# Optimization experiments

Hardware: AMD Instinct MI355X
Metric: run time of the kernel (lower is better)

## Reference

```python
import jax, jax.numpy as jnp
import numpy as np

BS = 4096
FD = 768   # feature_dim
PD = 500   # proj_dim
ZD = 300   # z_dim
R = 10     # retrieval_num
U = 10     # retrieval_user_num
N_PER = 3 + 2 * R + U  # 33 nodes per sample


def _lin(x, w, b):
    return x @ w.T + b


def _build_incidence(bs, r, u):
    # Faithful to get_hyper_edge_index_and_weight: 4 group edges per sample
    # plus R pair edges that (as in the original code) omit the batch bias,
    # i.e. always reference sample-0 nodes. dhg.Hypergraph dedups duplicate
    # edges, so the R pair edges appear once.
    n = 3 + 2 * r + u
    node_list, edge_list = [], []
    e = 0
    for b in range(bs):
        o = b * n
        groups = [
            list(range(o, o + 3)),
            list(range(o + 3, o + 3 + r)) + [o],
            list(range(o + 3 + r, o + 3 + 2 * r)) + [o + 1],
            list(range(o + 3 + 2 * r, o + n)) + [o + 2],
        ]
        for g in groups:
            node_list.extend(g)
            edge_list.extend([e] * len(g))
            e += 1
    for i in range(r):
        node_list.extend([3 + i, 3 + r + i])
        edge_list.extend([e, e])
        e += 1
    return np.asarray(node_list, np.int32), np.asarray(edge_list, np.int32), e


def setup_inputs() -> dict:
    key = jax.random.key(0)
    ks = jax.random.split(key, 32)

    def rn(k, shape, s=1.0):
        return jax.random.normal(k, shape, dtype=jnp.float32) * s

    inp = {
        "visual_feature": rn(ks[0], (BS, 1, FD)),
        "textual_feature": rn(ks[1], (BS, 1, FD)),
        "similarity": rn(ks[2], (BS, R)),
        "retrieved_visual_feature": rn(ks[3], (BS, R, 1, FD)),
        "retrieved_textual_feature": rn(ks[4], (BS, R, FD)),
        "retrieved_label": jax.random.uniform(ks[5], (BS, R, 1), dtype=jnp.float32),
        "user": rn(ks[6], (BS, FD)),
        "retrieved_user": rn(ks[7], (BS, U, FD)),
        "retrieved_user_similarity": rn(ks[8], (BS, U)),
        # learned params (0.02-scaled normal init)
        "vis_w": rn(ks[9], (PD, FD), 0.02), "vis_b": jnp.zeros((PD,), jnp.float32),
        "txt_w": rn(ks[10], (PD, FD), 0.02), "txt_b": jnp.zeros((PD,), jnp.float32),
        "usr_w": rn(ks[11], (PD, FD), 0.02), "usr_b": jnp.zeros((PD,), jnp.float32),
        "rvis_w": rn(ks[12], (PD, FD), 0.02), "rvis_b": jnp.zeros((PD,), jnp.float32),
        "rtxt_w": rn(ks[13], (PD, FD), 0.02), "rtxt_b": jnp.zeros((PD,), jnp.float32),
        "rusr_w": rn(ks[14], (PD, FD), 0.02), "rusr_b": jnp.zeros((PD,), jnp.float32),
        "hg_w": rn(ks[15], (ZD, PD), 0.02), "hg_b": jnp.zeros((ZD,), jnp.float32),
        "lbl_w": rn(ks[16], (ZD, 1), 0.02), "lbl_b": jnp.zeros((ZD,), jnp.float32),
        "p1_w": rn(ks[17], (800, ZD * 7), 0.02), "p1_b": jnp.zeros((800,), jnp.float32),
        "p2_w": rn(ks[18], (200, 800), 0.02), "p2_b": jnp.zeros((200,), jnp.float32),
        "p3_w": rn(ks[19], (1, 200), 0.02), "p3_b": jnp.zeros((1,), jnp.float32),
    }
    return inp


def reference(visual_feature, textual_feature, similarity, retrieved_visual_feature,
              retrieved_textual_feature, retrieved_label, user, retrieved_user,
              retrieved_user_similarity,
              vis_w, vis_b, txt_w, txt_b, usr_w, usr_b,
              rvis_w, rvis_b, rtxt_w, rtxt_b, rusr_w, rusr_b,
              hg_w, hg_b, lbl_w, lbl_b,
              p1_w, p1_b, p2_w, p2_b, p3_w, p3_b):
    bs = visual_feature.shape[0]
    # dense tanh embeddings -> per-sample node feature block [bs, 33, 500]
    t = jnp.tanh(_lin(textual_feature, txt_w, txt_b))
    v = jnp.tanh(_lin(visual_feature, vis_w, vis_b))
    u = jnp.tanh(_lin(user[:, None, :], usr_w, usr_b))
    rt = jnp.tanh(_lin(retrieved_textual_feature, rtxt_w, rtxt_b))
    rv = jnp.tanh(_lin(retrieved_visual_feature[:, :, 0, :], rvis_w, rvis_b))
    ru = jnp.tanh(_lin(retrieved_user, rusr_w, rusr_b))
    X = jnp.concatenate([t, v, u, rt, rv, ru], axis=1).reshape(-1, PD)  # [bs*33, 500]

    # hypergraph conv (HGNN+ layer, softmax_then_sum over unit incidence == mean)
    node_ids, edge_ids, E = _build_incidence(bs, R, U)  # static, built at trace time
    N = X.shape[0]
    Xt = _lin(X, hg_w, hg_b)  # theta: [N, 300]
    ones = jnp.ones(node_ids.shape[0], jnp.float32)
    deg_e = jax.ops.segment_sum(ones, edge_ids, num_segments=E)
    Y = jax.ops.segment_sum(Xt[node_ids], edge_ids, num_segments=E) / deg_e[:, None]
    deg_v = jax.ops.segment_sum(ones, node_ids, num_segments=N)
    Xo = jax.ops.segment_sum(Y[edge_ids], node_ids, num_segments=N) / deg_v[:, None]
    Xo = jax.nn.relu(Xo).reshape(bs, N_PER, ZD)

    # retrieval aggregation: softmax-weighted sums over retrieved sets
    sim = jax.nn.softmax(similarity, axis=1)                      # [bs, R]
    usim = jax.nn.softmax(retrieved_user_similarity, axis=1)      # [bs, U]
    rt_agg = jnp.einsum('br,brd->bd', sim, Xo[:, 3:3 + R, :])
    rv_agg = jnp.einsum('br,brd->bd', sim, Xo[:, 3 + R:3 + 2 * R, :])
    ru_agg = jnp.einsum('br,brd->bd', usim, Xo[:, 3 + 2 * R:3 + 2 * R + U, :])
    lbl_agg = jnp.einsum('br,bro->bo', sim, retrieved_label)      # [bs, 1]
    lbl_emb = jax.nn.relu(_lin(lbl_agg, lbl_w, lbl_b))            # [bs, 300]

    feat = jnp.concatenate(
        [Xo[:, 0, :], Xo[:, 1, :], Xo[:, 2, :], rv_agg, rt_agg, ru_agg, lbl_emb], axis=1)
    h = jax.nn.relu(_lin(feat, p1_w, p1_b))
    h = jax.nn.relu(_lin(h, p2_w, p2_b))
    out = jax.nn.sigmoid(_lin(h, p3_w, p3_b))  # [bs, 1]
    return out
```

## Files before the change

kernel.cpp:

```cpp
#include <hip/hip_runtime.h>
#include <math.h>

#define BS 4096
#define FD 768
#define PD 500
#define ZD 300
#define RNUM 10

typedef short bf16x8 __attribute__((ext_vector_type(8)));
typedef float f32x4 __attribute__((ext_vector_type(4)));

__device__ __forceinline__ unsigned int fbits(float f) {
  union { float f; unsigned int u; } v; v.f = f; return v.u;
}

__device__ __forceinline__ unsigned int pack2bf(float f0, float f1) {
  unsigned int u0 = fbits(f0) + 0x8000u;
  unsigned int u1 = fbits(f1) + 0x8000u;
  return __builtin_amdgcn_perm(u1, u0, 0x07060302u);
}

#define BM 128
#define BN 64
#define BK 16
#define TM 8
#define TN 4
template <int ACT>
__global__ __launch_bounds__(256) void gemm_kernel(
    const float* __restrict__ A, const float* __restrict__ W,
    const float* __restrict__ bias, float* __restrict__ C,
    int M, int N, int K) {
  __shared__ float As[BK][BM + 4];
  __shared__ float Bs[BK][BN + 4];
  const int m0 = blockIdx.x * BM;
  const int n0 = blockIdx.y * BN;
  const int tid = threadIdx.x;
  const int tx = tid & 15;
  const int ty = tid >> 4;
  float acc[TM][TN];
#pragma unroll
  for (int i = 0; i < TM; i++)
#pragma unroll
    for (int j = 0; j < TN; j++) acc[i][j] = 0.f;
  const int l_row = tid >> 2;
  const int l_k4 = (tid & 3) * 4;
  for (int k0 = 0; k0 < K; k0 += BK) {
#pragma unroll
    for (int half = 0; half < 2; ++half) {
      int m = m0 + l_row + half * 64;
      int k = k0 + l_k4;
      float4 v = make_float4(0.f, 0.f, 0.f, 0.f);
      if (m < M && k + 4 <= K) v = *(const float4*)(A + (size_t)m * K + k);
      As[l_k4 + 0][l_row + half * 64] = v.x;
      As[l_k4 + 1][l_row + half * 64] = v.y;
      As[l_k4 + 2][l_row + half * 64] = v.z;
      As[l_k4 + 3][l_row + half * 64] = v.w;
    }
    {
      int n = n0 + l_row;
      int k = k0 + l_k4;
      float4 v = make_float4(0.f, 0.f, 0.f, 0.f);
      if (n < N && k + 4 <= K) v = *(const float4*)(W + (size_t)n * K + k);
      Bs[l_k4 + 0][l_row] = v.x;
      Bs[l_k4 + 1][l_row] = v.y;
      Bs[l_k4 + 2][l_row] = v.z;
      Bs[l_k4 + 3][l_row] = v.w;
    }
    __syncthreads();
#pragma unroll
    for (int k = 0; k < BK; k++) {
      float a[TM], b[TN];
#pragma unroll
      for (int i = 0; i < TM; i++) a[i] = As[k][ty * TM + i];
#pragma unroll
      for (int j = 0; j < TN; j++) b[j] = Bs[k][tx * TN + j];
#pragma unroll
      for (int i = 0; i < TM; i++)
#pragma unroll
        for (int j = 0; j < TN; j++) acc[i][j] += a[i] * b[j];
    }
    __syncthreads();
  }
#pragma unroll
  for (int i = 0; i < TM; i++) {
    int m = m0 + ty * TM + i;
    if (m >= M) continue;
#pragma unroll
    for (int j = 0; j < TN; j++) {
      int n = n0 + tx * TN + j;
      if (n >= N) continue;
      float v = acc[i][j] + bias[n];
      if (ACT == 1) v = fmaxf(v, 0.f);
      C[(size_t)m * N + n] = v;
    }
  }
}

__global__ __launch_bounds__(256) void padcast(
    const float* __restrict__ src, unsigned short* __restrict__ dst,
    int rs, int cs, int rd, int cd) {
  int i = blockIdx.x * 256 + threadIdx.x;
  if (i >= rd * cd) return;
  int r = i / cd, c = i - r * cd;
  float v = (r < rs && c < cs) ? src[(size_t)r * cs + c] : 0.f;
  dst[i] = (unsigned short)((fbits(v) + 0x8000u) >> 16);
}


template <int ACT>
__global__ __launch_bounds__(256) void mfma_gemm(
    const float* __restrict__ A, int lda, int Ka,
    const unsigned short* __restrict__ B, int Kp,
    const float* __restrict__ bias, float* __restrict__ C, int Nout) {
  __shared__ unsigned short ldsA[128 * 32];
  __shared__ unsigned short ldsB[128 * 32];
  const int tid = threadIdx.x;
  const int n0 = blockIdx.x * 128;
  const int m0 = blockIdx.y * 128;

  const int arow = tid >> 1;
  const int ahalf = (tid & 1) << 4;
  const int ag = (tid & 1) << 1;
  const int aswz = (arow >> 1) & 3;
  unsigned short* awp0 = &ldsA[((size_t)arow * 4 + ((ag | 0) ^ aswz)) * 8];
  unsigned short* awp1 = &ldsA[((size_t)arow * 4 + ((ag | 1) ^ aswz)) * 8];
  const float* aptr = A + (size_t)(m0 + arow) * lda;

  unsigned short* bwp0 = &ldsB[((size_t)arow * 4 + ((ag | 0) ^ aswz)) * 8];
  unsigned short* bwp1 = &ldsB[((size_t)arow * 4 + ((ag | 1) ^ aswz)) * 8];
  const unsigned short* bptr = B + (size_t)(n0 + arow) * Kp + ag * 8;

  const int lane = tid & 63;
  const int wave = tid >> 6;
  const int wm = (wave >> 1) << 6;
  const int wn = (wave & 1) << 6;
  const int r16 = lane & 15;
  const int kq = lane >> 4;

  const unsigned short* afp[4];
  const unsigned short* bfp[4];
#pragma unroll
  for (int i = 0; i < 4; i++) {
    int rowA = wm + i * 16 + r16;
    afp[i] = &ldsA[((size_t)rowA * 4 + (kq ^ ((rowA >> 1) & 3))) * 8];
    int rowB = wn + i * 16 + r16;
    bfp[i] = &ldsB[((size_t)rowB * 4 + (kq ^ ((rowB >> 1) & 3))) * 8];
  }

  f32x4 acc[4][4] = {};

  for (int k0 = 0; k0 < Kp; k0 += 32) {
    float4 f[4];
#pragma unroll
    for (int q = 0; q < 4; q++) {
      int k = k0 + ahalf + q * 4;
      if (k < Ka) f[q] = *(const float4*)(aptr + k);
      else f[q] = make_float4(0.f, 0.f, 0.f, 0.f);
    }
    uint4 w0, w1;
    w0.x = pack2bf(f[0].x, f[0].y); w0.y = pack2bf(f[0].z, f[0].w);
    w0.z = pack2bf(f[1].x, f[1].y); w0.w = pack2bf(f[1].z, f[1].w);
    w1.x = pack2bf(f[2].x, f[2].y); w1.y = pack2bf(f[2].z, f[2].w);
    w1.z = pack2bf(f[3].x, f[3].y); w1.w = pack2bf(f[3].z, f[3].w);
    uint4 bv0 = *(const uint4*)(bptr + k0);
    uint4 bv1 = *(const uint4*)(bptr + k0 + 8);
    *(uint4*)awp0 = w0;
    *(uint4*)awp1 = w1;
    *(uint4*)bwp0 = bv0;
    *(uint4*)bwp1 = bv1;
    __syncthreads();
    bf16x8 a[4], b[4];
#pragma unroll
    for (int i = 0; i < 4; i++) a[i] = *(const bf16x8*)afp[i];
#pragma unroll
    for (int i = 0; i < 4; i++) b[i] = *(const bf16x8*)bfp[i];
#pragma unroll
    for (int i = 0; i < 4; i++)
#pragma unroll
      for (int j = 0; j < 4; j++)
        acc[i][j] = __builtin_amdgcn_mfma_f32_16x16x32_bf16(a[i], b[j], acc[i][j], 0, 0, 0);
    __syncthreads();
  }

#pragma unroll
  for (int j = 0; j < 4; j++) {
    int n = n0 + wn + j * 16 + r16;
    if (n >= Nout) continue;
    float bi = bias[n];
#pragma unroll
    for (int i = 0; i < 4; i++) {
#pragma unroll
      for (int r = 0; r < 4; r++) {
        int m = m0 + wm + i * 16 + kq * 4 + r;
        float v = acc[i][j][r] + bi;
        if (ACT == 1) v = fmaxf(v, 0.f);
        C[(size_t)m * Nout + n] = v;
      }
    }
  }
}

struct EmbedArgs {
  const float* A[6];
  const float* bias[6];
};

__global__ __launch_bounds__(256) void embed_mfma(
    EmbedArgs ea, const unsigned short* __restrict__ Wbf,
    float* __restrict__ S, float* __restrict__ E0) {
  __shared__ unsigned short ldsA[128 * 32];
  __shared__ unsigned short ldsB[128 * 32];
  const int tid = threadIdx.x;
  const int n0 = blockIdx.x * 128;
  const int m0 = blockIdx.y * 128;

  int g, base;
  if (m0 < 4096) { g = 0; base = 0; }
  else if (m0 < 8192) { g = 1; base = 4096; }
  else if (m0 < 12288) { g = 2; base = 8192; }
  else if (m0 < 53248) { g = 3; base = 12288; }
  else if (m0 < 94208) { g = 4; base = 53248; }
  else { g = 5; base = 94208; }

  const int arow = tid >> 1;
  const int ahalf = (tid & 1) << 4;
  const int ag = (tid & 1) << 1;
  const int aswz = (arow >> 1) & 3;
  unsigned short* awp0 = &ldsA[((size_t)arow * 4 + ((ag | 0) ^ aswz)) * 8];
  unsigned short* awp1 = &ldsA[((size_t)arow * 4 + ((ag | 1) ^ aswz)) * 8];
  const float* aptr = ea.A[g] + (size_t)(m0 - base + arow) * FD;

  unsigned short* bwp0 = &ldsB[((size_t)arow * 4 + ((ag | 0) ^ aswz)) * 8];
  unsigned short* bwp1 = &ldsB[((size_t)arow * 4 + ((ag | 1) ^ aswz)) * 8];
  const unsigned short* bptr =
      Wbf + (size_t)g * 512 * FD + (size_t)(n0 + arow) * FD + ag * 8;

  const int lane = tid & 63;
  const int wave = tid >> 6;
  const int wm = (wave >> 1) << 6;
  const int wn = (wave & 1) << 6;
  const int r16 = lane & 15;
  const int kq = lane >> 4;

  const unsigned short* afp[4];
  const unsigned short* bfp[4];
#pragma unroll
  for (int i = 0; i < 4; i++) {
    int rowA = wm + i * 16 + r16;
    afp[i] = &ldsA[((size_t)rowA * 4 + (kq ^ ((rowA >> 1) & 3))) * 8];
    int rowB = wn + i * 16 + r16;
    bfp[i] = &ldsB[((size_t)rowB * 4 + (kq ^ ((rowB >> 1) & 3))) * 8];
  }

  f32x4 acc[4][4] = {};

  for (int k0 = 0; k0 < FD; k0 += 32) {
    float4 f[4];
#pragma unroll
    for (int q = 0; q < 4; q++) f[q] = *(const float4*)(aptr + k0 + ahalf + q * 4);
    uint4 w0, w1;
    w0.x = pack2bf(f[0].x, f[0].y); w0.y = pack2bf(f[0].z, f[0].w);
    w0.z = pack2bf(f[1].x, f[1].y); w0.w = pack2bf(f[1].z, f[1].w);
    w1.x = pack2bf(f[2].x, f[2].y); w1.y = pack2bf(f[2].z, f[2].w);
    w1.z = pack2bf(f[3].x, f[3].y); w1.w = pack2bf(f[3].z, f[3].w);
    uint4 bv0 = *(const uint4*)(bptr + k0);
    uint4 bv1 = *(const uint4*)(bptr + k0 + 8);
    *(uint4*)awp0 = w0;
    *(uint4*)awp1 = w1;
    *(uint4*)bwp0 = bv0;
    *(uint4*)bwp1 = bv1;
    __syncthreads();
    bf16x8 a[4], b[4];
#pragma unroll
    for (int i = 0; i < 4; i++) a[i] = *(const bf16x8*)afp[i];
#pragma unroll
    for (int i = 0; i < 4; i++) b[i] = *(const bf16x8*)bfp[i];
#pragma unroll
    for (int i = 0; i < 4; i++)
#pragma unroll
      for (int j = 0; j < 4; j++)
        acc[i][j] = __builtin_amdgcn_mfma_f32_16x16x32_bf16(a[i], b[j], acc[i][j], 0, 0, 0);
    __syncthreads();
  }

  const float* bias = ea.bias[g];
#pragma unroll
  for (int j = 0; j < 4; j++) {
    int n = n0 + wn + j * 16 + r16;
    if (n >= PD) continue;
    float bi = bias[n];
#pragma unroll
    for (int i = 0; i < 4; i++) {
#pragma unroll
      for (int r = 0; r < 4; r++) {
        int m = m0 + wm + i * 16 + kq * 4 + r;
        int rl = m - base;
        float v = tanhf(acc[i][j][r] + bi);
        if (g < 3) {
          S[((size_t)g * BS + rl) * PD + n] = v;
        } else {
          int bb = rl / 10;
          int rr = rl - bb * 10;
          atomicAdd(&S[((size_t)g * BS + bb) * PD + n], v);
          if (g != 5 && bb == 0) E0[((size_t)(g - 3) * 10 + rr) * PD + n] = v;
        }
      }
    }
  }
}

__global__ __launch_bounds__(256) void means_kernel(
    const float* __restrict__ S, float* __restrict__ Mn) {
  const int total = 4 * BS * PD;
  for (int i = blockIdx.x * blockDim.x + threadIdx.x; i < total;
       i += gridDim.x * blockDim.x) {
    int m = i / PD;
    int k = i - m * PD;
    int b = m >> 2, e = m & 3;
    float v;
    const size_t o = (size_t)b * PD + k;
    if (e == 0)
      v = (S[o] + S[(size_t)BS * PD + o] + S[2 * (size_t)BS * PD + o]) * (1.f / 3.f);
    else if (e == 1)
      v = (S[3 * (size_t)BS * PD + o] + S[o]) * (1.f / 11.f);
    else if (e == 2)
      v = (S[4 * (size_t)BS * PD + o] + S[(size_t)BS * PD + o]) * (1.f / 11.f);
    else
      v = (S[5 * (size_t)BS * PD + o] + S[2 * (size_t)BS * PD + o]) * (1.f / 11.f);
    Mn[i] = v;
  }
}

__global__ __launch_bounds__(256) void xte_kernel(
    const float* __restrict__ E0, const float* __restrict__ hg_w,
    const float* __restrict__ hg_b, float* __restrict__ XtE) {
  const int i = blockIdx.x;
  __shared__ float row[PD];
  for (int k = threadIdx.x; k < PD; k += 256) row[k] = E0[(size_t)i * PD + k];
  __syncthreads();
  for (int n = threadIdx.x; n < ZD; n += 256) {
    float s = 0.f;
    const float* w = hg_w + (size_t)n * PD;
    for (int k = 0; k < PD; k++) s += row[k] * w[k];
    XtE[(size_t)i * ZD + n] = s + hg_b[n];
  }
}

__global__ __launch_bounds__(256) void feat_kernel(
    const float* __restrict__ Y, const float* __restrict__ XtE,
    const float* __restrict__ sim_in, const float* __restrict__ label,
    const float* __restrict__ lbl_w, const float* __restrict__ lbl_b,
    float* __restrict__ feat) {
  const int b = blockIdx.x;
  __shared__ float w[RNUM];
  __shared__ float lbl_agg_s;
  if (threadIdx.x == 0) {
    float s[RNUM], mx = -1e30f;
    for (int r = 0; r < RNUM; r++) {
      s[r] = sim_in[(size_t)b * RNUM + r];
      mx = fmaxf(mx, s[r]);
    }
    float sum = 0.f;
    for (int r = 0; r < RNUM; r++) { s[r] = expf(s[r] - mx); sum += s[r]; }
    float la = 0.f;
    for (int r = 0; r < RNUM; r++) {
      w[r] = s[r] / sum;
      la += w[r] * label[(size_t)b * RNUM + r];
    }
    lbl_agg_s = la;
  }
  __syncthreads();
  const float* Yb = Y + (size_t)b * 4 * ZD;
  float* fb = feat + (size_t)b * 7 * ZD;
  const float la = lbl_agg_s;
  for (int n = threadIdx.x; n < ZD; n += blockDim.x) {
    float y0 = Yb[n], y1 = Yb[ZD + n], y2 = Yb[2 * ZD + n], y3 = Yb[3 * ZD + n];
    fb[n] = fmaxf(0.5f * (y0 + y1), 0.f);
    fb[ZD + n] = fmaxf(0.5f * (y0 + y2), 0.f);
    fb[2 * ZD + n] = fmaxf(0.5f * (y0 + y3), 0.f);
    float rv, rt;
    if (b == 0) {
      rv = 0.f; rt = 0.f;
      for (int r = 0; r < RNUM; r++) {
        float yp = 0.5f * (XtE[(size_t)r * ZD + n] + XtE[(size_t)(10 + r) * ZD + n]);
        rt += w[r] * fmaxf(0.5f * (y1 + yp), 0.f);
        rv += w[r] * fmaxf(0.5f * (y2 + yp), 0.f);
      }
    } else {
      rt = fmaxf(y1, 0.f);
      rv = fmaxf(y2, 0.f);
    }
    fb[3 * ZD + n] = rv;
    fb[4 * ZD + n] = rt;
    fb[5 * ZD + n] = fmaxf(y3, 0.f);
    fb[6 * ZD + n] = fmaxf(la * lbl_w[n] + lbl_b[n], 0.f);
  }
}

__global__ __launch_bounds__(256) void head_kernel(
    const float* __restrict__ h2, const float* __restrict__ p3_w,
    const float* __restrict__ p3_b, float* __restrict__ out) {
  const int wave = (blockIdx.x * blockDim.x + threadIdx.x) >> 6;
  const int lane = threadIdx.x & 63;
  if (wave >= BS) return;
  const float* row = h2 + (size_t)wave * 200;
  float s = 0.f;
  for (int k = lane; k < 200; k += 64) s += row[k] * p3_w[k];
#pragma unroll
  for (int off = 32; off; off >>= 1) s += __shfl_down(s, off, 64);
  if (lane == 0) out[wave] = 1.f / (1.f + expf(-(s + p3_b[0])));
}

extern "C" void kernel_launch(void* const* d_in, const int* in_sizes, int n_in,
                              void* d_out, int out_size, void* d_ws,
                              size_t ws_size, hipStream_t stream) {
  (void)in_sizes; (void)n_in; (void)out_size; (void)ws_size;

  const float* visual = (const float*)d_in[0];
  const float* textual = (const float*)d_in[1];
  const float* similarity = (const float*)d_in[2];
  const float* r_visual = (const float*)d_in[3];
  const float* r_textual = (const float*)d_in[4];
  const float* r_label = (const float*)d_in[5];
  const float* user = (const float*)d_in[6];
  const float* r_user = (const float*)d_in[7];
  const float* vis_w = (const float*)d_in[9];
  const float* vis_b = (const float*)d_in[10];
  const float* txt_w = (const float*)d_in[11];
  const float* txt_b = (const float*)d_in[12];
  const float* usr_w = (const float*)d_in[13];
  const float* usr_b = (const float*)d_in[14];
  const float* rvis_w = (const float*)d_in[15];
  const float* rvis_b = (const float*)d_in[16];
  const float* rtxt_w = (const float*)d_in[17];
  const float* rtxt_b = (const float*)d_in[18];
  const float* rusr_w = (const float*)d_in[19];
  const float* rusr_b = (const float*)d_in[20];
  const float* hg_w = (const float*)d_in[21];
  const float* hg_b = (const float*)d_in[22];
  const float* lbl_w = (const float*)d_in[23];
  const float* lbl_b = (const float*)d_in[24];
  const float* p1_w = (const float*)d_in[25];
  const float* p1_b = (const float*)d_in[26];
  const float* p2_w = (const float*)d_in[27];
  const float* p2_b = (const float*)d_in[28];
  const float* p3_w = (const float*)d_in[29];
  const float* p3_b = (const float*)d_in[30];
  float* out = (float*)d_out;

  float* ws = (float*)d_ws;
  float* S = ws;
  float* E0 = S + (size_t)6 * BS * PD;
  float* XtE = E0 + 20 * PD;
  float* Mn = XtE + 20 * ZD;
  float* Y = Mn + (size_t)4 * BS * PD;
  float* feat = Y + (size_t)4 * BS * ZD;
  float* h1 = feat + (size_t)BS * 7 * ZD;
  float* h2 = h1 + (size_t)BS * 800;
  unsigned short* Wbf = (unsigned short*)(h2 + (size_t)BS * 200);
  unsigned short* hgwbf = Wbf + (size_t)6 * 512 * FD;
  unsigned short* p1wbf = hgwbf + (size_t)384 * 512;

  const float* ew[6] = {txt_w, vis_w, usr_w, rtxt_w, rvis_w, rusr_w};
  for (int g = 0; g < 6; g++) {
    padcast<<<(512 * FD + 255) / 256, 256, 0, stream>>>(
        ew[g], Wbf + (size_t)g * 512 * FD, PD, FD, 512, FD);
  }
  padcast<<<(384 * 512 + 255) / 256, 256, 0, stream>>>(hg_w, hgwbf, ZD, PD, 384, 512);
  padcast<<<(896 * 2112 + 255) / 256, 256, 0, stream>>>(p1_w, p1wbf, 800, 2100, 896, 2112);

  hipMemsetAsync(S + (size_t)3 * BS * PD, 0, (size_t)3 * BS * PD * sizeof(float),
                 stream);

  EmbedArgs ea;
  ea.A[0] = textual;  ea.bias[0] = txt_b;
  ea.A[1] = visual;   ea.bias[1] = vis_b;
  ea.A[2] = user;     ea.bias[2] = usr_b;
  ea.A[3] = r_textual; ea.bias[3] = rtxt_b;
  ea.A[4] = r_visual;  ea.bias[4] = rvis_b;
  ea.A[5] = r_user;    ea.bias[5] = rusr_b;

  embed_mfma<<<dim3(4, 135168 / 128), 256, 0, stream>>>(ea, Wbf, S, E0);
  xte_kernel<<<20, 256, 0, stream>>>(E0, hg_w, hg_b, XtE);
  means_kernel<<<4096, 256, 0, stream>>>(S, Mn);
  mfma_gemm<0><<<dim3(3, 16384 / 128), 256, 0, stream>>>(
      Mn, PD, PD, hgwbf, 512, hg_b, Y, ZD);
  feat_kernel<<<BS, 256, 0, stream>>>(Y, XtE, similarity, r_label, lbl_w, lbl_b,
                                      feat);
  mfma_gemm<1><<<dim3(7, BS / 128), 256, 0, stream>>>(
      feat, 2100, 2100, p1wbf, 2112, p1_b, h1, 800);
  gemm_kernel<1><<<dim3(BS / BM, (200 + BN - 1) / BN), 256, 0, stream>>>(
      h1, p2_w, p2_b, h2, BS, 200, 800);
  head_kernel<<<BS * 64 / 256, 256, 0, stream>>>(h2, p3_w, p3_b, out);
}
```

Baseline: 1.304 ms.

## Double-buffer LDS in MFMA GEMMs, reduce retrieval epilogue in LDS, batch weight casts

Both MFMA GEMM kernels now use double-buffered shared memory with a single barrier per k-step, so the global loads for the next tile overlap the MFMA work on the current one. Launch bounds also ask for three blocks per CU. The embedding epilogue for retrieved groups stages the tanh outputs in LDS and sums each sample's 10 rows there, writing each sum directly and using atomics only for samples that straddle a tile boundary, instead of issuing one atomicAdd per element. The six weight padcast launches are merged into one launch. The trade-off is doubled LDS per block, extra barriers in the epilogue, and added register pressure.

```diff
diff --git a/kernel.cpp b/kernel.cpp
--- a/kernel.cpp
+++ b/kernel.cpp
@@ -6,6 +6,7 @@
 #define PD 500
 #define ZD 300
 #define RNUM 10
+#define LBUF (128 * 32)
 
 typedef short bf16x8 __attribute__((ext_vector_type(8)));
 typedef float f32x4 __attribute__((ext_vector_type(4)));
@@ -106,14 +107,22 @@
   dst[i] = (unsigned short)((fbits(v) + 0x8000u) >> 16);
 }
 
+struct W6 { const float* p[6]; };
+__global__ __launch_bounds__(256) void padcast6(W6 w, unsigned short* __restrict__ dst) {
+  const int g = blockIdx.y;
+  int i = blockIdx.x * 256 + threadIdx.x;
+  int r = i / FD, c = i - r * FD;
+  float v = (r < PD) ? w.p[g][(size_t)r * FD + c] : 0.f;
+  dst[(size_t)g * 512 * FD + i] = (unsigned short)((fbits(v) + 0x8000u) >> 16);
+}
+
 
 template <int ACT>
-__global__ __launch_bounds__(256) void mfma_gemm(
+__global__ __launch_bounds__(256, 3) void mfma_gemm(
     const float* __restrict__ A, int lda, int Ka,
     const unsigned short* __restrict__ B, int Kp,
     const float* __restrict__ bias, float* __restrict__ C, int Nout) {
-  __shared__ unsigned short ldsA[128 * 32];
-  __shared__ unsigned short ldsB[128 * 32];
+  __shared__ unsigned short lds[2][2 * LBUF];
   const int tid = threadIdx.x;
   const int n0 = blockIdx.x * 128;
   const int m0 = blockIdx.y * 128;
@@ -122,12 +131,9 @@
   const int ahalf = (tid & 1) << 4;
   const int ag = (tid & 1) << 1;
   const int aswz = (arow >> 1) & 3;
-  unsigned short* awp0 = &ldsA[((size_t)arow * 4 + ((ag | 0) ^ aswz)) * 8];
-  unsigned short* awp1 = &ldsA[((size_t)arow * 4 + ((ag | 1) ^ aswz)) * 8];
+  const int awo0 = (arow * 4 + ((ag | 0) ^ aswz)) * 8;
+  const int awo1 = (arow * 4 + ((ag | 1) ^ aswz)) * 8;
   const float* aptr = A + (size_t)(m0 + arow) * lda;
-
-  unsigned short* bwp0 = &ldsB[((size_t)arow * 4 + ((ag | 0) ^ aswz)) * 8];
-  unsigned short* bwp1 = &ldsB[((size_t)arow * 4 + ((ag | 1) ^ aswz)) * 8];
   const unsigned short* bptr = B + (size_t)(n0 + arow) * Kp + ag * 8;
 
   const int lane = tid & 63;
@@ -137,49 +143,62 @@
   const int r16 = lane & 15;
   const int kq = lane >> 4;
 
-  const unsigned short* afp[4];
-  const unsigned short* bfp[4];
+  int afo[4], bfo[4];
 #pragma unroll
   for (int i = 0; i < 4; i++) {
     int rowA = wm + i * 16 + r16;
-    afp[i] = &ldsA[((size_t)rowA * 4 + (kq ^ ((rowA >> 1) & 3))) * 8];
+    afo[i] = (rowA * 4 + (kq ^ ((rowA >> 1) & 3))) * 8;
     int rowB = wn + i * 16 + r16;
-    bfp[i] = &ldsB[((size_t)rowB * 4 + (kq ^ ((rowB >> 1) & 3))) * 8];
+    bfo[i] = LBUF + (rowB * 4 + (kq ^ ((rowB >> 1) & 3))) * 8;
   }
 
   f32x4 acc[4][4] = {};
-
-  for (int k0 = 0; k0 < Kp; k0 += 32) {
-    float4 f[4];
+  float4 f[4];
+  uint4 bv0, bv1;
+
+  auto gload = [&](int k0) {
 #pragma unroll
     for (int q = 0; q < 4; q++) {
       int k = k0 + ahalf + q * 4;
       if (k < Ka) f[q] = *(const float4*)(aptr + k);
       else f[q] = make_float4(0.f, 0.f, 0.f, 0.f);
     }
+    bv0 = *(const uint4*)(bptr + k0);
+    bv1 = *(const uint4*)(bptr + k0 + 8);
+  };
+  auto pstore = [&](unsigned short* L) {
     uint4 w0, w1;
     w0.x = pack2bf(f[0].x, f[0].y); w0.y = pack2bf(f[0].z, f[0].w);
     w0.z = pack2bf(f[1].x, f[1].y); w0.w = pack2bf(f[1].z, f[1].w);
     w1.x = pack2bf(f[2].x, f[2].y); w1.y = pack2bf(f[2].z, f[2].w);
     w1.z = pack2bf(f[3].x, f[3].y); w1.w = pack2bf(f[3].z, f[3].w);
-    uint4 bv0 = *(const uint4*)(bptr + k0);
-    uint4 bv1 = *(const uint4*)(bptr + k0 + 8);
-    *(uint4*)awp0 = w0;
-    *(uint4*)awp1 = w1;
-    *(uint4*)bwp0 = bv0;
-    *(uint4*)bwp1 = bv1;
+    *(uint4*)(L + awo0) = w0;
+    *(uint4*)(L + awo1) = w1;
+    *(uint4*)(L + LBUF + awo0) = bv0;
+    *(uint4*)(L + LBUF + awo1) = bv1;
+  };
+
+  gload(0);
+  pstore(lds[0]);
+  int cur = 0;
+  for (int k0 = 32;; k0 += 32) {
     __syncthreads();
+    const bool more = (k0 < Kp);
+    if (more) gload(k0);
+    const unsigned short* Lc = lds[cur];
     bf16x8 a[4], b[4];
 #pragma unroll
-    for (int i = 0; i < 4; i++) a[i] = *(const bf16x8*)afp[i];
-#pragma unroll
-    for (int i = 0; i < 4; i++) b[i] = *(const bf16x8*)bfp[i];
+    for (int i = 0; i < 4; i++) a[i] = *(const bf16x8*)(Lc + afo[i]);
+#pragma unroll
+    for (int i = 0; i < 4; i++) b[i] = *(const bf16x8*)(Lc + bfo[i]);
 #pragma unroll
     for (int i = 0; i < 4; i++)
 #pragma unroll
       for (int j = 0; j < 4; j++)
         acc[i][j] = __builtin_amdgcn_mfma_f32_16x16x32_bf16(a[i], b[j], acc[i][j], 0, 0, 0);
-    __syncthreads();
+    if (!more) break;
+    cur ^= 1;
+    pstore(lds[cur]);
   }
 
 #pragma unroll
@@ -205,11 +224,10 @@
   const float* bias[6];
 };
 
-__global__ __launch_bounds__(256) void embed_mfma(
+__global__ __launch_bounds__(256, 3) void embed_mfma(
     EmbedArgs ea, const unsigned short* __restrict__ Wbf,
     float* __restrict__ S, float* __restrict__ E0) {
-  __shared__ unsigned short ldsA[128 * 32];
-  __shared__ unsigned short ldsB[128 * 32];
+  __shared__ unsigned short lds[2][2 * LBUF];
   const int tid = threadIdx.x;
   const int n0 = blockIdx.x * 128;
   const int m0 = blockIdx.y * 128;
@@ -226,12 +244,9 @@
   const int ahalf = (tid & 1) << 4;
   const int ag = (tid & 1) << 1;
   const int aswz = (arow >> 1) & 3;
-  unsigned short* awp0 = &ldsA[((size_t)arow * 4 + ((ag | 0) ^ aswz)) * 8];
-  unsigned short* awp1 = &ldsA[((size_t)arow * 4 + ((ag | 1) ^ aswz)) * 8];
+  const int awo0 = (arow * 4 + ((ag | 0) ^ aswz)) * 8;
+  const int awo1 = (arow * 4 + ((ag | 1) ^ aswz)) * 8;
   const float* aptr = ea.A[g] + (size_t)(m0 - base + arow) * FD;
-
-  unsigned short* bwp0 = &ldsB[((size_t)arow * 4 + ((ag | 0) ^ aswz)) * 8];
-  unsigned short* bwp1 = &ldsB[((size_t)arow * 4 + ((ag | 1) ^ aswz)) * 8];
   const unsigned short* bptr =
       Wbf + (size_t)g * 512 * FD + (size_t)(n0 + arow) * FD + ag * 8;
 
@@ -242,68 +257,130 @@
   const int r16 = lane & 15;
   const int kq = lane >> 4;
 
-  const unsigned short* afp[4];
-  const unsigned short* bfp[4];
+  int afo[4], bfo[4];
 #pragma unroll
   for (int i = 0; i < 4; i++) {
     int rowA = wm + i * 16 + r16;
-    afp[i] = &ldsA[((size_t)rowA * 4 + (kq ^ ((rowA >> 1) & 3))) * 8];
+    afo[i] = (rowA * 4 + (kq ^ ((rowA >> 1) & 3))) * 8;
     int rowB = wn + i * 16 + r16;
-    bfp[i] = &ldsB[((size_t)rowB * 4 + (kq ^ ((rowB >> 1) & 3))) * 8];
+    bfo[i] = LBUF + (rowB * 4 + (kq ^ ((rowB >> 1) & 3))) * 8;
   }
 
   f32x4 acc[4][4] = {};
-
-  for (int k0 = 0; k0 < FD; k0 += 32) {
-    float4 f[4];
+  float4 f[4];
+  uint4 bv0, bv1;
+
+  auto gload = [&](int k0) {
 #pragma unroll
     for (int q = 0; q < 4; q++) f[q] = *(const float4*)(aptr + k0 + ahalf + q * 4);
+    bv0 = *(const uint4*)(bptr + k0);
+    bv1 = *(const uint4*)(bptr + k0 + 8);
+  };
+  auto pstore = [&](unsigned short* L) {
     uint4 w0, w1;
     w0.x = pack2bf(f[0].x, f[0].y); w0.y = pack2bf(f[0].z, f[0].w);
     w0.z = pack2bf(f[1].x, f[1].y); w0.w = pack2bf(f[1].z, f[1].w);
     w1.x = pack2bf(f[2].x, f[2].y); w1.y = pack2bf(f[2].z, f[2].w);
     w1.z = pack2bf(f[3].x, f[3].y); w1.w = pack2bf(f[3].z, f[3].w);
-    uint4 bv0 = *(const uint4*)(bptr + k0);
-    uint4 bv1 = *(const uint4*)(bptr + k0 + 8);
-    *(uint4*)awp0 = w0;
-    *(uint4*)awp1 = w1;
-    *(uint4*)bwp0 = bv0;
-    *(uint4*)bwp1 = bv1;
+    *(uint4*)(L + awo0) = w0;
+    *(uint4*)(L + awo1) = w1;
+    *(uint4*)(L + LBUF + awo0) = bv0;
+    *(uint4*)(L + LBUF + awo1) = bv1;
+  };
+
+  gload(0);
+  pstore(lds[0]);
+  int cur = 0;
+  for (int k0 = 32;; k0 += 32) {
     __syncthreads();
+    const bool more = (k0 < FD);
+    if (more) gload(k0);
+    const unsigned short* Lc = lds[cur];
     bf16x8 a[4], b[4];
 #pragma unroll
-    for (int i = 0; i < 4; i++) a[i] = *(const bf16x8*)afp[i];
-#pragma unroll
-    for (int i = 0; i < 4; i++) b[i] = *(const bf16x8*)bfp[i];
+    for (int i = 0; i < 4; i++) a[i] = *(const bf16x8*)(Lc + afo[i]);
+#pragma unroll
+    for (int i = 0; i < 4; i++) b[i] = *(const bf16x8*)(Lc + bfo[i]);
 #pragma unroll
     for (int i = 0; i < 4; i++)
 #pragma unroll
       for (int j = 0; j < 4; j++)
         acc[i][j] = __builtin_amdgcn_mfma_f32_16x16x32_bf16(a[i], b[j], acc[i][j], 0, 0, 0);
-    __syncthreads();
+    if (!more) break;
+    cur ^= 1;
+    pstore(lds[cur]);
   }
 
   const float* bias = ea.bias[g];
-#pragma unroll
-  for (int j = 0; j < 4; j++) {
-    int n = n0 + wn + j * 16 + r16;
-    if (n >= PD) continue;
-    float bi = bias[n];
-#pragma unroll
-    for (int i = 0; i < 4; i++) {
-#pragma unroll
-      for (int r = 0; r < 4; r++) {
-        int m = m0 + wm + i * 16 + kq * 4 + r;
-        int rl = m - base;
-        float v = tanhf(acc[i][j][r] + bi);
-        if (g < 3) {
-          S[((size_t)g * BS + rl) * PD + n] = v;
-        } else {
-          int bb = rl / 10;
-          int rr = rl - bb * 10;
-          atomicAdd(&S[((size_t)g * BS + bb) * PD + n], v);
-          if (g != 5 && bb == 0) E0[((size_t)(g - 3) * 10 + rr) * PD + n] = v;
+  const int base_r = m0 - base;
+
+  if (g < 3) {
+#pragma unroll
+    for (int j = 0; j < 4; j++) {
+      int n = n0 + wn + j * 16 + r16;
+      if (n >= PD) continue;
+      float bi = bias[n];
+#pragma unroll
+      for (int i = 0; i < 4; i++)
+#pragma unroll
+        for (int r = 0; r < 4; r++) {
+          int row = wm + i * 16 + kq * 4 + r;
+          S[((size_t)g * BS + base_r + row) * PD + n] = tanhf(acc[i][j][r] + bi);
         }
+    }
+  } else {
+    if (g != 5 && base_r == 0 && wm == 0) {
+#pragma unroll
+      for (int j = 0; j < 4; j++) {
+        int n = n0 + wn + j * 16 + r16;
+        if (n >= PD) continue;
+        float bi = bias[n];
+#pragma unroll
+        for (int r = 0; r < 4; r++) {
+          int row = kq * 4 + r;
+          if (row < 10)
+            E0[((size_t)(g - 3) * 10 + row) * PD + n] = tanhf(acc[0][j][r] + bi);
+        }
+      }
+    }
+    const int s0 = base_r / 10;
+    const int ns = (base_r + 127) / 10 - s0 + 1;
+    float* red = (float*)lds;
+    for (int c = 0; c < 4; c++) {
+      __syncthreads();
+      int jb = (c * 32 - wn) / 16;
+      if (jb >= 0 && jb < 4) {
+#pragma unroll
+        for (int jj = 0; jj < 2; jj++) {
+          int j = jb + jj;
+          int col = wn + j * 16 + r16;
+          int cc = col - c * 32;
+          int n = n0 + col;
+          float bi = (n < PD) ? bias[n] : 0.f;
+#pragma unroll
+          for (int i = 0; i < 4; i++)
+#pragma unroll
+            for (int r = 0; r < 4; r++) {
+              int row = wm + i * 16 + kq * 4 + r;
+              red[row * 32 + cc] = tanhf(acc[i][j][r] + bi);
+            }
+        }
+      }
+      __syncthreads();
+      for (int p = tid; p < ns * 32; p += 256) {
+        int ls = p >> 5, cc = p & 31;
+        int n = n0 + c * 32 + cc;
+        if (n >= PD) continue;
+        int s = s0 + ls;
+        int rlo = s * 10 - base_r;
+        int rhi = rlo + 10;
+        if (rlo < 0) rlo = 0;
+        if (rhi > 128) rhi = 128;
+        float sum = 0.f;
+        for (int r = rlo; r < rhi; r++) sum += red[r * 32 + cc];
+        size_t idx = ((size_t)g * BS + s) * PD + n;
+        if (rhi - rlo == 10) S[idx] = sum;
+        else atomicAdd(&S[idx], sum);
       }
     }
   }
@@ -461,11 +538,10 @@
   unsigned short* hgwbf = Wbf + (size_t)6 * 512 * FD;
   unsigned short* p1wbf = hgwbf + (size_t)384 * 512;
 
-  const float* ew[6] = {txt_w, vis_w, usr_w, rtxt_w, rvis_w, rusr_w};
-  for (int g = 0; g < 6; g++) {
-    padcast<<<(512 * FD + 255) / 256, 256, 0, stream>>>(
-        ew[g], Wbf + (size_t)g * 512 * FD, PD, FD, 512, FD);
-  }
+  W6 w6;
+  w6.p[0] = txt_w; w6.p[1] = vis_w; w6.p[2] = usr_w;
+  w6.p[3] = rtxt_w; w6.p[4] = rvis_w; w6.p[5] = rusr_w;
+  padcast6<<<dim3(512 * FD / 256, 6), 256, 0, stream>>>(w6, Wbf);
   padcast<<<(384 * 512 + 255) / 256, 256, 0, stream>>>(hg_w, hgwbf, ZD, PD, 384, 512);
   padcast<<<(896 * 2112 + 255) / 256, 256, 0, stream>>>(p1_w, p1wbf, 800, 2100, 896, 2112);
 
```

After: 3.023 ms. 132% more time.
